# Kernel optimization log

Measured on AMD Instinct MI355X. Metric: run time of the kernel, lower is better.

The kernel has to match this reference:

```python
import jax, jax.numpy as jnp
import numpy as np

B, L, E, H, G, W, D = 2, 4096, 1024, 16, 2, 256, 64  # D = E // H; KV dim = E // (H // G)


def _rope(q, k, sin, cos):
    # Matches torch apply_rotary_pos_emb: split even/odd, concat halves (not interleaved).
    qe, qo = q[..., ::2], q[..., 1::2]
    ke, ko = k[..., ::2], k[..., 1::2]
    q_rot = jnp.concatenate([qe * cos - qo * sin, qe * sin + qo * cos], axis=-1)
    k_rot = jnp.concatenate([ke * cos - ko * sin, ke * sin + ko * cos], axis=-1)
    return q_rot, k_rot


def setup_inputs() -> dict:
    key = jax.random.key(0)
    ks = jax.random.split(key, 8)
    kv_dim = E // (H // G)  # 128
    s = 0.02
    return {
        "x": jax.random.normal(ks[0], (B, L, E), jnp.float32),
        "Wq1": jax.random.normal(ks[1], (E, E), jnp.float32) * s,
        "Wq2": jax.random.normal(ks[2], (E, E), jnp.float32) * s,
        "Wk1": jax.random.normal(ks[3], (E, kv_dim), jnp.float32) * s,
        "Wk2": jax.random.normal(ks[4], (E, kv_dim), jnp.float32) * s,
        "Wv": jax.random.normal(ks[5], (E, kv_dim), jnp.float32) * s,
        "Wout": jax.random.normal(ks[6], (E, E), jnp.float32) * s,
        "bout": jnp.zeros((E,), jnp.float32),
        "lq1": jnp.full((D,), 0.1, jnp.float32),
        "lk1": jnp.full((D,), 0.1, jnp.float32),
        "lq2": jnp.full((D,), -0.1, jnp.float32),
        "lk2": jnp.full((D,), -0.1, jnp.float32),
    }


def reference(x, Wq1, Wq2, Wk1, Wk2, Wv, Wout, bout, lq1, lk1, lq2, lk2):
    Bx, Lx, _ = x.shape  # Lx is a multiple of W -> pad_l = 0
    lambda_init = 0.8

    # Projections -> (B, H, L, D) and (B, G, L, D)
    q1 = (x @ Wq1).reshape(Bx, Lx, H, D).transpose(0, 2, 1, 3)
    q2 = (x @ Wq2).reshape(Bx, Lx, H, D).transpose(0, 2, 1, 3)
    k1 = (x @ Wk1).reshape(Bx, Lx, G, D).transpose(0, 2, 1, 3)
    k2 = (x @ Wk2).reshape(Bx, Lx, G, D).transpose(0, 2, 1, 3)
    v = (x @ Wv).reshape(Bx, Lx, G, D).transpose(0, 2, 1, 3)

    # RoPE tables (L, D/2) broadcast as (1, 1, L, D/2)
    pos = jnp.arange(Lx, dtype=jnp.float32)[:, None]
    div = jnp.exp(jnp.arange(0, D, 2, dtype=jnp.float32) * (-np.log(10000.0) / D))
    sin = jnp.sin(pos * div)[None, None]
    cos = jnp.cos(pos * div)[None, None]
    q1, k1 = _rope(q1, k1, sin, cos)
    q2, k2 = _rope(q2, k2, sin, cos)

    # Differential lambda (scalar), clamped to [0.1, 0.9]
    lam = jnp.clip(jnp.exp(lq1 @ lk1) - jnp.exp(lq2 @ lk2) + lambda_init, 0.1, 0.9)

    # KV repeat via torch .repeat(1, H//G, 1, 1): tiling -> head h uses group h % G
    gidx = jnp.arange(H) % G
    k1h, k2h, vh = k1[:, gidx], k2[:, gidx], v[:, gidx]  # (B, H, L, D)

    # Overlapping windows, stride W//2
    nw = (Lx - W) // (W // 2) + 1
    idx = jnp.arange(nw)[:, None] * (W // 2) + jnp.arange(W)[None, :]  # (nw, W)

    def win(t):
        return t[:, :, idx, :]  # (B, H, nw, W, D)

    scale = 1.0 / np.sqrt(D)

    def attn(qw, kw, vw):
        sc = jnp.einsum('bhnqd,bhnkd->bhnqk', qw, kw) * scale
        p = jax.nn.softmax(sc, axis=-1)  # bidirectional -> no causal mask
        return jnp.einsum('bhnqk,bhnkd->bhnqd', p, vw)

    a1 = attn(win(q1), win(k1h), win(vh))
    a2 = attn(win(q2), win(k2h), win(vh))
    a = a1 - lam * a2  # (B, H, nw, W, D)

    # Concatenate windows along seq (dim 2), transpose, flatten heads, trim to L
    a = a.reshape(Bx, H, nw * W, D).transpose(0, 2, 1, 3).reshape(Bx, nw * W, E)
    a = a[:, :Lx]
    return a @ Wout + bout
```

## Files before the change

### kernel.cpp

```cpp
#include <hip/hip_runtime.h>

#define SS    2176

typedef __bf16 bf16x8 __attribute__((ext_vector_type(8)));
typedef float floatx4 __attribute__((ext_vector_type(4)));
typedef const __attribute__((address_space(1))) void* as1cv;
typedef __attribute__((address_space(3))) void* as3v;

typedef uint4 __attribute__((may_alias, aligned(16))) uint4a;
typedef uint2 __attribute__((may_alias, aligned(8)))  uint2a;
typedef unsigned int __attribute__((may_alias)) uinta;

__device__ __forceinline__ float bf2f(unsigned short u) {
  unsigned int x = ((unsigned int)u) << 16;
  return __builtin_bit_cast(float, x);
}
__device__ __forceinline__ unsigned short f2bf(float f) {
  unsigned int u = __builtin_bit_cast(unsigned int, f);
  u = (u + 0x7fffu + ((u >> 16) & 1u)) >> 16;
  return (unsigned short)u;
}
#if __has_builtin(__builtin_amdgcn_cvt_pk_bf16_f32)
typedef __bf16 bf16x2 __attribute__((ext_vector_type(2)));
__device__ __forceinline__ unsigned int pk2bf(float a, float b) {
  bf16x2 r = __builtin_amdgcn_cvt_pk_bf16_f32(a, b);
  return __builtin_bit_cast(unsigned int, r);
}
#else
__device__ __forceinline__ unsigned int pk2bf(float a, float b) {
  return (unsigned int)f2bf(a) | ((unsigned int)f2bf(b) << 16);
}
#endif
__device__ __forceinline__ float fexp2(float x) {
#if __has_builtin(__builtin_amdgcn_exp2f)
  return __builtin_amdgcn_exp2f(x);
#else
  return exp2f(x);
#endif
}
__device__ __forceinline__ bf16x8 ld_frag(const unsigned short* p) {
  uint4 u = *(const uint4a*)p;
  return __builtin_bit_cast(bf16x8, u);
}
__device__ __forceinline__ bool sniff_bf16(const void* lq1) {
  return ((*(const uinta*)lq1) >> 16) == 0x3DCDu;
}
__device__ __forceinline__ float ldin(const void* p, int i, bool bf) {
  return bf ? bf2f(((const unsigned short*)p)[i]) : ((const float*)p)[i];
}

__global__ __launch_bounds__(256) void prep_kernel(
    const void* __restrict__ x,
    const void* __restrict__ Wq1, const void* __restrict__ Wq2,
    const void* __restrict__ Wk1, const void* __restrict__ Wk2,
    const void* __restrict__ Wv,  const void* __restrict__ Wout,
    const void* __restrict__ lq1, const void* __restrict__ lk1,
    const void* __restrict__ lq2, const void* __restrict__ lk2,
    unsigned short* __restrict__ WT, unsigned short* __restrict__ WoutT,
    float2* __restrict__ SC, float* __restrict__ lam_out,
    unsigned short* __restrict__ Xb)
{
  int bid = blockIdx.x, tid = threadIdx.x;
  bool bf = sniff_bf16(lq1);
  if (bid >= 1137) {
    int i = (bid - 1137) * 2048 + tid * 8;
    int r = i >> 10, c = i & 1023;
    size_t sidx = (size_t)(r + (r >= SS ? 1920 : 0)) * 1024 + c;
    if (bf) {
      *(uint4a*)(Xb + i) = *(const uint4a*)((const unsigned short*)x + sidx);
    } else {
      const float* xf = (const float*)x + sidx;
      uint4 o;
      o.x = pk2bf(xf[0], xf[1]); o.y = pk2bf(xf[2], xf[3]);
      o.z = pk2bf(xf[4], xf[5]); o.w = pk2bf(xf[6], xf[7]);
      *(uint4a*)(Xb + i) = o;
    }
  } else if (bid < 864) {
    __shared__ unsigned short T[64][80];
    const void* src; unsigned short* dst;
    int width, nloc, n0, k0;
    if (bid < 608) {
      n0 = (bid >> 4) * 64; k0 = (bid & 15) * 64; dst = WT;
      if      (n0 < 1024) { src = Wq1; width = 1024; nloc = n0; }
      else if (n0 < 2048) { src = Wq2; width = 1024; nloc = n0 - 1024; }
      else if (n0 < 2176) { src = Wk1; width = 128;  nloc = n0 - 2048; }
      else if (n0 < 2304) { src = Wk2; width = 128;  nloc = n0 - 2176; }
      else                { src = Wv;  width = 128;  nloc = n0 - 2304; }
    } else {
      int id = bid - 608;
      n0 = (id >> 4) * 64; k0 = (id & 15) * 64; dst = WoutT;
      src = Wout; width = 1024; nloc = n0;
    }
    for (int e = tid; e < 4096; e += 256) {
      int rr = e >> 6, cc = e & 63;
      size_t idx = (size_t)(k0 + rr) * width + nloc + cc;
      T[rr][cc] = bf ? ((const unsigned short*)src)[idx]
                     : f2bf(((const float*)src)[idx]);
    }
    __syncthreads();
#pragma unroll
    for (int it = 0; it < 2; ++it) {
      int rn = (tid >> 3) + it * 32;
      int ck = (tid & 7) * 8;
      unsigned short tmp[8] __attribute__((aligned(16)));
#pragma unroll
      for (int j = 0; j < 8; ++j) tmp[j] = T[ck + j][rn];
      *(uint4a*)(dst + (size_t)(n0 + rn) * 1024 + k0 + ck) = *(const uint4a*)tmp;
    }
  } else if (bid < 1136) {
    int idx = (bid - 864) * 256 + tid;
    int s = idx >> 5, j = idx & 31;
    float freq = expf(-(float)j * 0.28782313662425572f);
    float ang = (float)s * freq;
    SC[idx] = make_float2(sinf(ang), cosf(ang));
  } else {
    if (tid < 64) {
      float a = ldin(lq1, tid, bf) * ldin(lk1, tid, bf);
      float c = ldin(lq2, tid, bf) * ldin(lk2, tid, bf);
#pragma unroll
      for (int m = 32; m >= 1; m >>= 1) {
        a += __shfl_xor(a, m);
        c += __shfl_xor(c, m);
      }
      if (tid == 0) {
        float lam = expf(a) - expf(c) + 0.8f;
        lam = fminf(0.9f, fmaxf(0.1f, lam));
        *lam_out = lam;
      }
    }
  }
}

__global__ __launch_bounds__(256) void proj_gemm(
    const unsigned short* __restrict__ Xb, const unsigned short* __restrict__ WT,
    const float2* __restrict__ SC,
    unsigned short* __restrict__ Q1R, unsigned short* __restrict__ Q2R,
    unsigned short* __restrict__ K1R, unsigned short* __restrict__ K2R,
    unsigned short* __restrict__ VTg)
{
  __shared__ unsigned short As[128 * 32];
  __shared__ unsigned short Bs[128 * 32];
  int tid = threadIdx.x;
  int w = tid >> 6, lane = tid & 63, quad = lane >> 4, l15 = lane & 15;
  int wr = w >> 1, wc = w & 1;
  int n0 = blockIdx.x * 128, m0 = blockIdx.y * 128;
  int b = (m0 >= SS) ? 1 : 0;
  int srow = w * 32 + (lane >> 2);
  int scol = (((lane & 3) ^ ((lane >> 3) & 3))) * 8;
  int rch  = (quad ^ ((l15 >> 1) & 3)) * 8;

  floatx4 acc[4][4];
#pragma unroll
  for (int i = 0; i < 4; ++i)
#pragma unroll
    for (int j = 0; j < 4; ++j) acc[i][j] = (floatx4){0.f, 0.f, 0.f, 0.f};

  unsigned short* lA = As + (size_t)(w * 32) * 32;
  unsigned short* lB = Bs + (size_t)(w * 32) * 32;
  const unsigned short* gA = Xb + (size_t)(m0 + srow) * 1024 + scol;
  const unsigned short* gB = WT + (size_t)(n0 + srow) * 1024 + scol;

  for (int it = 0; it < 32; ++it) {
    int k0 = it * 32;
    __builtin_amdgcn_global_load_lds((as1cv)(gA + k0), (as3v)lA, 16, 0, 0);
    __builtin_amdgcn_global_load_lds((as1cv)(gA + 16 * 1024 + k0), (as3v)(lA + 16 * 32), 16, 0, 0);
    __builtin_amdgcn_global_load_lds((as1cv)(gB + k0), (as3v)lB, 16, 0, 0);
    __builtin_amdgcn_global_load_lds((as1cv)(gB + 16 * 1024 + k0), (as3v)(lB + 16 * 32), 16, 0, 0);
    __syncthreads();
    bf16x8 af[4], bfm[4];
#pragma unroll
    for (int rt = 0; rt < 4; ++rt)
      af[rt] = ld_frag(As + (size_t)(wr * 64 + rt * 16 + l15) * 32 + rch);
#pragma unroll
    for (int nt = 0; nt < 4; ++nt)
      bfm[nt] = ld_frag(Bs + (size_t)(wc * 64 + nt * 16 + l15) * 32 + rch);
#pragma unroll
    for (int rt = 0; rt < 4; ++rt)
#pragma unroll
      for (int nt = 0; nt < 4; ++nt)
        acc[rt][nt] = __builtin_amdgcn_mfma_f32_16x16x32_bf16(af[rt], bfm[nt], acc[rt][nt], 0, 0, 0);
    __syncthreads();
  }

  int seg, segbase;
  if      (n0 < 1024) { seg = 0; segbase = 0; }
  else if (n0 < 2048) { seg = 1; segbase = 1024; }
  else if (n0 < 2176) { seg = 2; segbase = 2048; }
  else if (n0 < 2304) { seg = 3; segbase = 2176; }
  else                { seg = 4; segbase = 2304; }
  int rb = m0 + wr * 64;

  if (seg == 4) {
#pragma unroll
    for (int rt = 0; rt < 4; ++rt) {
      int r = rb + rt * 16 + quad * 4;
      int s = r - b * SS;
#pragma unroll
      for (int nt = 0; nt < 4; ++nt) {
        int cs = n0 - segbase + wc * 64 + nt * 16 + l15;
        int gi = cs >> 6, dd = cs & 63;
        uint2 pk;
        pk.x = pk2bf(acc[rt][nt].x, acc[rt][nt].y);
        pk.y = pk2bf(acc[rt][nt].z, acc[rt][nt].w);
        *(uint2a*)(VTg + ((size_t)(b * 2 + gi) * 64 + dd) * SS + s) = pk;
      }
    }
  } else {
    unsigned short* dst = (seg == 0) ? Q1R : (seg == 1) ? Q2R : (seg == 2) ? K1R : K2R;
    bool isq = (seg <= 1);
    float oscale = isq ? 0.18033688011112042f : 1.0f;
#pragma unroll
    for (int rt = 0; rt < 4; ++rt) {
#pragma unroll
      for (int nt = 0; nt < 4; ++nt) {
        int cs = n0 - segbase + wc * 64 + nt * 16 + l15;
        int hh = cs >> 6, dd = cs & 63, j = dd >> 1, par = dd & 1;
        size_t tb = isq ? ((size_t)(b * 16 + hh) * SS) : ((size_t)(b * 2 + hh) * SS);
        int dloc = j + par * 32;
#pragma unroll
        for (int rg = 0; rg < 4; ++rg) {
          float v = acc[rt][nt][rg];
          float pv = __shfl_xor(v, 1);
          int r = rb + rt * 16 + quad * 4 + rg;
          int s = r - b * SS;
          float2 sc = SC[s * 32 + j];
          float o = par ? (pv * sc.x + v * sc.y) : (v * sc.y - pv * sc.x);
          dst[(tb + s) * 64 + dloc] = f2bf(o * oscale);
        }
      }
    }
  }
}

__global__ __launch_bounds__(512) void attn_kernel(
    const unsigned short* __restrict__ Q1R, const unsigned short* __restrict__ Q2R,
    const unsigned short* __restrict__ K1R, const unsigned short* __restrict__ K2R,
    const unsigned short* __restrict__ VTg, const float* __restrict__ lamp,
    unsigned short* __restrict__ Abuf)
{
  __shared__ unsigned short K1s[256 * 64];
  __shared__ unsigned short K2s[256 * 64];
  __shared__ unsigned short VTs[64 * 256];
  __shared__ unsigned short P[8][2][32 * 40];
  int nx = blockIdx.x, hp = blockIdx.y, b = blockIdx.z;
  int n = nx >> 1, qh = nx & 1;
  int g = hp & 1, hpair = hp >> 1;
  int tid = threadIdx.x, w = tid >> 6, lane = tid & 63, quad = lane >> 4, l15 = lane & 15;
  int wq = w & 3;
  int h = g + 4 * hpair + 2 * (w >> 2);
  int s0 = n * 128;
  int qbase = s0 + qh * 128 + wq * 32;

  const unsigned short* q1b = Q1R + (size_t)(b * 16 + h) * SS * 64;
  const unsigned short* q2b = Q2R + (size_t)(b * 16 + h) * SS * 64;
  const unsigned short* k1w = K1R + ((size_t)(b * 2 + g) * SS + s0) * 64;
  const unsigned short* k2w = K2R + ((size_t)(b * 2 + g) * SS + s0) * 64;
  const unsigned short* vtw = VTg + (size_t)(b * 2 + g) * 64 * SS + s0;

#pragma unroll
  for (int i = 0; i < 4; ++i) {
    int r = i * 64 + (tid >> 3);
    int cg = (tid & 7) ^ (r & 7);
    __builtin_amdgcn_global_load_lds((as1cv)(k1w + r * 64 + cg * 8),
        (as3v)(K1s + i * 4096 + tid * 8), 16, 0, 0);
    __builtin_amdgcn_global_load_lds((as1cv)(k2w + r * 64 + cg * 8),
        (as3v)(K2s + i * 4096 + tid * 8), 16, 0, 0);
  }
#pragma unroll
  for (int i = 0; i < 4; ++i) {
    int d = i * 16 + (tid >> 5);
    int cg = (tid & 31) ^ (d & 7);
    __builtin_amdgcn_global_load_lds((as1cv)(vtw + (size_t)d * SS + cg * 8),
        (as3v)(VTs + i * 4096 + tid * 8), 16, 0, 0);
  }

  bf16x8 q1f[2][2], q2f[2][2];
#pragma unroll
  for (int rt = 0; rt < 2; ++rt) {
    int sq = qbase + rt * 16 + l15;
#pragma unroll
    for (int kt = 0; kt < 2; ++kt) {
      q1f[rt][kt] = ld_frag(q1b + (size_t)sq * 64 + kt * 32 + quad * 8);
      q2f[rt][kt] = ld_frag(q2b + (size_t)sq * 64 + kt * 32 + quad * 8);
    }
  }
  float lam = *lamp;

  floatx4 O1[2][4], O2[2][4];
  float l1s[2] = {0.f, 0.f}, l2s[2] = {0.f, 0.f};
#pragma unroll
  for (int rt = 0; rt < 2; ++rt)
#pragma unroll
    for (int dt = 0; dt < 4; ++dt) {
      O1[rt][dt] = (floatx4){0.f, 0.f, 0.f, 0.f};
      O2[rt][dt] = (floatx4){0.f, 0.f, 0.f, 0.f};
    }

  __syncthreads();

  for (int c = 0; c < 4; ++c) {
#pragma unroll
    for (int ntp = 0; ntp < 2; ++ntp) {
      int kbl = c * 64 + ntp * 32;
      bf16x8 k1f[2][2], k2f[2][2], vb[4];
#pragma unroll
      for (int ntl = 0; ntl < 2; ++ntl) {
        int kl = kbl + ntl * 16 + l15;
#pragma unroll
        for (int kt = 0; kt < 2; ++kt) {
          int slot = (kt * 4 + quad) ^ (kl & 7);
          k1f[ntl][kt] = ld_frag(K1s + kl * 64 + slot * 8);
          k2f[ntl][kt] = ld_frag(K2s + kl * 64 + slot * 8);
        }
      }
#pragma unroll
      for (int dt = 0; dt < 4; ++dt) {
        int d = dt * 16 + l15;
        int slot = ((kbl >> 3) + quad) ^ (d & 7);
        vb[dt] = ld_frag(VTs + d * 256 + slot * 8);
      }

#pragma unroll
      for (int rt = 0; rt < 2; ++rt)
#pragma unroll
        for (int ntl = 0; ntl < 2; ++ntl) {
          floatx4 sa = (floatx4){0.f, 0.f, 0.f, 0.f};
          sa = __builtin_amdgcn_mfma_f32_16x16x32_bf16(k1f[ntl][0], q1f[rt][0], sa, 0, 0, 0);
          sa = __builtin_amdgcn_mfma_f32_16x16x32_bf16(k1f[ntl][1], q1f[rt][1], sa, 0, 0, 0);
          floatx4 pe;
          pe.x = fexp2(sa.x); pe.y = fexp2(sa.y);
          pe.z = fexp2(sa.z); pe.w = fexp2(sa.w);
          l1s[rt] += (pe.x + pe.y) + (pe.z + pe.w);
          uint2 dw; dw.x = pk2bf(pe.x, pe.y); dw.y = pk2bf(pe.z, pe.w);
          *(uint2a*)&P[w][0][(rt * 16 + l15) * 40 + ntl * 16 + quad * 4] = dw;
        }
#pragma unroll
      for (int rt = 0; rt < 2; ++rt)
#pragma unroll
        for (int ntl = 0; ntl < 2; ++ntl) {
          floatx4 sa = (floatx4){0.f, 0.f, 0.f, 0.f};
          sa = __builtin_amdgcn_mfma_f32_16x16x32_bf16(k2f[ntl][0], q2f[rt][0], sa, 0, 0, 0);
          sa = __builtin_amdgcn_mfma_f32_16x16x32_bf16(k2f[ntl][1], q2f[rt][1], sa, 0, 0, 0);
          floatx4 pe;
          pe.x = fexp2(sa.x); pe.y = fexp2(sa.y);
          pe.z = fexp2(sa.z); pe.w = fexp2(sa.w);
          l2s[rt] += (pe.x + pe.y) + (pe.z + pe.w);
          uint2 dw; dw.x = pk2bf(pe.x, pe.y); dw.y = pk2bf(pe.z, pe.w);
          *(uint2a*)&P[w][1][(rt * 16 + l15) * 40 + ntl * 16 + quad * 4] = dw;
        }
#pragma unroll
      for (int rt = 0; rt < 2; ++rt) {
        bf16x8 pa = ld_frag(&P[w][0][(rt * 16 + l15) * 40 + quad * 8]);
#pragma unroll
        for (int dt = 0; dt < 4; ++dt)
          O1[rt][dt] = __builtin_amdgcn_mfma_f32_16x16x32_bf16(pa, vb[dt], O1[rt][dt], 0, 0, 0);
      }
#pragma unroll
      for (int rt = 0; rt < 2; ++rt) {
        bf16x8 pa = ld_frag(&P[w][1][(rt * 16 + l15) * 40 + quad * 8]);
#pragma unroll
        for (int dt = 0; dt < 4; ++dt)
          O2[rt][dt] = __builtin_amdgcn_mfma_f32_16x16x32_bf16(pa, vb[dt], O2[rt][dt], 0, 0, 0);
      }
    }
  }

#pragma unroll
  for (int rt = 0; rt < 2; ++rt) {
    l1s[rt] += __shfl_xor(l1s[rt], 16); l1s[rt] += __shfl_xor(l1s[rt], 32);
    l2s[rt] += __shfl_xor(l2s[rt], 16); l2s[rt] += __shfl_xor(l2s[rt], 32);
  }

#pragma unroll
  for (int rt = 0; rt < 2; ++rt) {
    floatx4 r1, r2;
#pragma unroll
    for (int rg = 0; rg < 4; ++rg) {
      int src = (lane & 48) | (quad * 4 + rg);
      r1[rg] = 1.f / __shfl(l1s[rt], src);
      r2[rg] = lam / __shfl(l2s[rt], src);
    }
#pragma unroll
    for (int dt = 0; dt < 4; ++dt) {
#pragma unroll
      for (int rg = 0; rg < 4; ++rg) {
        float v = O1[rt][dt][rg] * r1[rg] - O2[rt][dt][rg] * r2[rg];
        int prow = n * 256 + qh * 128 + wq * 32 + rt * 16 + quad * 4 + rg;
        int col = h * 64 + dt * 16 + l15;
        Abuf[((size_t)b * 4096 + prow) * 1024 + col] = f2bf(v);
      }
    }
  }
}

__global__ __launch_bounds__(256) void out_gemm(
    const unsigned short* __restrict__ A, const unsigned short* __restrict__ WoutT,
    const void* __restrict__ bout, const void* __restrict__ lq1,
    void* __restrict__ out)
{
  __shared__ unsigned short As[128 * 32];
  __shared__ unsigned short Bs[128 * 32];
  int tid = threadIdx.x;
  int w = tid >> 6, lane = tid & 63, quad = lane >> 4, l15 = lane & 15;
  int wr = w >> 1, wc = w & 1;
  int n0 = blockIdx.x * 128, m0 = blockIdx.y * 128;
  int srow = w * 32 + (lane >> 2);
  int scol = (((lane & 3) ^ ((lane >> 3) & 3))) * 8;
  int rch  = (quad ^ ((l15 >> 1) & 3)) * 8;
  bool bf = sniff_bf16(lq1);

  floatx4 acc[4][4];
#pragma unroll
  for (int i = 0; i < 4; ++i)
#pragma unroll
    for (int j = 0; j < 4; ++j) acc[i][j] = (floatx4){0.f, 0.f, 0.f, 0.f};

  unsigned short* lA = As + (size_t)(w * 32) * 32;
  unsigned short* lB = Bs + (size_t)(w * 32) * 32;
  const unsigned short* gA = A + (size_t)(m0 + srow) * 1024 + scol;
  const unsigned short* gB = WoutT + (size_t)(n0 + srow) * 1024 + scol;

  for (int it = 0; it < 32; ++it) {
    int k0 = it * 32;
    __builtin_amdgcn_global_load_lds((as1cv)(gA + k0), (as3v)lA, 16, 0, 0);
    __builtin_amdgcn_global_load_lds((as1cv)(gA + 16 * 1024 + k0), (as3v)(lA + 16 * 32), 16, 0, 0);
    __builtin_amdgcn_global_load_lds((as1cv)(gB + k0), (as3v)lB, 16, 0, 0);
    __builtin_amdgcn_global_load_lds((as1cv)(gB + 16 * 1024 + k0), (as3v)(lB + 16 * 32), 16, 0, 0);
    __syncthreads();
    bf16x8 af[4], bfm[4];
#pragma unroll
    for (int rt = 0; rt < 4; ++rt)
      af[rt] = ld_frag(As + (size_t)(wr * 64 + rt * 16 + l15) * 32 + rch);
#pragma unroll
    for (int nt = 0; nt < 4; ++nt)
      bfm[nt] = ld_frag(Bs + (size_t)(wc * 64 + nt * 16 + l15) * 32 + rch);
#pragma unroll
    for (int rt = 0; rt < 4; ++rt)
#pragma unroll
      for (int nt = 0; nt < 4; ++nt)
        acc[rt][nt] = __builtin_amdgcn_mfma_f32_16x16x32_bf16(af[rt], bfm[nt], acc[rt][nt], 0, 0, 0);
    __syncthreads();
  }

#pragma unroll
  for (int rt = 0; rt < 4; ++rt)
#pragma unroll
    for (int nt = 0; nt < 4; ++nt) {
      int cc = n0 + wc * 64 + nt * 16 + l15;
      float bias = ldin(bout, cc, bf);
#pragma unroll
      for (int rg = 0; rg < 4; ++rg) {
        int r = m0 + wr * 64 + rt * 16 + quad * 4 + rg;
        float v = acc[rt][nt][rg] + bias;
        if (bf) ((unsigned short*)out)[(size_t)r * 1024 + cc] = f2bf(v);
        else    ((float*)out)[(size_t)r * 1024 + cc] = v;
      }
    }
}

extern "C" void kernel_launch(void* const* d_in, const int* in_sizes, int n_in,
                              void* d_out, int out_size, void* d_ws, size_t ws_size,
                              hipStream_t stream) {
  (void)in_sizes; (void)n_in; (void)out_size; (void)ws_size;
  const void* x    = d_in[0];
  const void* Wq1  = d_in[1];
  const void* Wq2  = d_in[2];
  const void* Wk1  = d_in[3];
  const void* Wk2  = d_in[4];
  const void* Wv   = d_in[5];
  const void* Wout = d_in[6];
  const void* bout = d_in[7];
  const void* lq1  = d_in[8];
  const void* lk1  = d_in[9];
  const void* lq2  = d_in[10];
  const void* lk2  = d_in[11];

  char* ws = (char*)d_ws;
  unsigned short* WT    = (unsigned short*)(ws + 0);
  unsigned short* WoutT = (unsigned short*)(ws + 4980736);
  float2*         SC    = (float2*)(ws + 7077888);
  float*          lam   = (float*)(ws + 7634944);
  unsigned short* Q1R   = (unsigned short*)(ws + 7635200);
  unsigned short* Q2R   = (unsigned short*)(ws + 16548096);
  unsigned short* K1R   = (unsigned short*)(ws + 25460992);
  unsigned short* K2R   = (unsigned short*)(ws + 26575104);
  unsigned short* VTg   = (unsigned short*)(ws + 27689216);
  unsigned short* Abuf  = (unsigned short*)(ws + 28803328);
  unsigned short* Xb    = (unsigned short*)(ws + 45580544);

  prep_kernel<<<3313, 256, 0, stream>>>(x, Wq1, Wq2, Wk1, Wk2, Wv, Wout,
                                        lq1, lk1, lq2, lk2, WT, WoutT, SC, lam, Xb);
  proj_gemm<<<dim3(19, 34), 256, 0, stream>>>(Xb, WT, SC, Q1R, Q2R, K1R, K2R, VTg);
  attn_kernel<<<dim3(32, 8, 2), 512, 0, stream>>>(Q1R, Q2R, K1R, K2R, VTg, lam, Abuf);
  out_gemm<<<dim3(8, 64), 256, 0, stream>>>(Abuf, WoutT, bout, lq1, (unsigned short*)d_out);
}
```

Before: 222.8 us.

## Double-buffer LDS tiles in projection and output GEMMs to overlap loads with MFMA

The projection and output GEMM kernels now keep two LDS stages for A and B. The global-to-LDS load for the next K-tile is issued before the MFMA work on the current tile, with a prologue that preloads the first tile. The goal is to hide global memory latency behind matrix compute instead of stalling on a barrier right after each load. This doubles LDS use per block, which could reduce occupancy, and it relies on the trailing per-iteration barrier to wait for the async loads.

```diff
diff --git a/kernel.cpp b/kernel.cpp
--- a/kernel.cpp
+++ b/kernel.cpp
@@ -138,8 +138,8 @@
     unsigned short* __restrict__ K1R, unsigned short* __restrict__ K2R,
     unsigned short* __restrict__ VTg)
 {
-  __shared__ unsigned short As[128 * 32];
-  __shared__ unsigned short Bs[128 * 32];
+  __shared__ unsigned short As[2][128 * 32];
+  __shared__ unsigned short Bs[2][128 * 32];
   int tid = threadIdx.x;
   int w = tid >> 6, lane = tid & 63, quad = lane >> 4, l15 = lane & 15;
   int wr = w >> 1, wc = w & 1;
@@ -155,25 +155,32 @@
 #pragma unroll
     for (int j = 0; j < 4; ++j) acc[i][j] = (floatx4){0.f, 0.f, 0.f, 0.f};
 
-  unsigned short* lA = As + (size_t)(w * 32) * 32;
-  unsigned short* lB = Bs + (size_t)(w * 32) * 32;
+  int wb = w * 32 * 32;
   const unsigned short* gA = Xb + (size_t)(m0 + srow) * 1024 + scol;
   const unsigned short* gB = WT + (size_t)(n0 + srow) * 1024 + scol;
 
+  __builtin_amdgcn_global_load_lds((as1cv)gA, (as3v)(As[0] + wb), 16, 0, 0);
+  __builtin_amdgcn_global_load_lds((as1cv)(gA + 16 * 1024), (as3v)(As[0] + wb + 16 * 32), 16, 0, 0);
+  __builtin_amdgcn_global_load_lds((as1cv)gB, (as3v)(Bs[0] + wb), 16, 0, 0);
+  __builtin_amdgcn_global_load_lds((as1cv)(gB + 16 * 1024), (as3v)(Bs[0] + wb + 16 * 32), 16, 0, 0);
+  __syncthreads();
+
   for (int it = 0; it < 32; ++it) {
-    int k0 = it * 32;
-    __builtin_amdgcn_global_load_lds((as1cv)(gA + k0), (as3v)lA, 16, 0, 0);
-    __builtin_amdgcn_global_load_lds((as1cv)(gA + 16 * 1024 + k0), (as3v)(lA + 16 * 32), 16, 0, 0);
-    __builtin_amdgcn_global_load_lds((as1cv)(gB + k0), (as3v)lB, 16, 0, 0);
-    __builtin_amdgcn_global_load_lds((as1cv)(gB + 16 * 1024 + k0), (as3v)(lB + 16 * 32), 16, 0, 0);
-    __syncthreads();
+    int cur = it & 1;
+    if (it < 31) {
+      int k1 = (it + 1) * 32;
+      __builtin_amdgcn_global_load_lds((as1cv)(gA + k1), (as3v)(As[cur ^ 1] + wb), 16, 0, 0);
+      __builtin_amdgcn_global_load_lds((as1cv)(gA + 16 * 1024 + k1), (as3v)(As[cur ^ 1] + wb + 16 * 32), 16, 0, 0);
+      __builtin_amdgcn_global_load_lds((as1cv)(gB + k1), (as3v)(Bs[cur ^ 1] + wb), 16, 0, 0);
+      __builtin_amdgcn_global_load_lds((as1cv)(gB + 16 * 1024 + k1), (as3v)(Bs[cur ^ 1] + wb + 16 * 32), 16, 0, 0);
+    }
     bf16x8 af[4], bfm[4];
 #pragma unroll
     for (int rt = 0; rt < 4; ++rt)
-      af[rt] = ld_frag(As + (size_t)(wr * 64 + rt * 16 + l15) * 32 + rch);
+      af[rt] = ld_frag(As[cur] + (size_t)(wr * 64 + rt * 16 + l15) * 32 + rch);
 #pragma unroll
     for (int nt = 0; nt < 4; ++nt)
-      bfm[nt] = ld_frag(Bs + (size_t)(wc * 64 + nt * 16 + l15) * 32 + rch);
+      bfm[nt] = ld_frag(Bs[cur] + (size_t)(wc * 64 + nt * 16 + l15) * 32 + rch);
 #pragma unroll
     for (int rt = 0; rt < 4; ++rt)
 #pragma unroll
@@ -398,8 +405,8 @@
     const void* __restrict__ bout, const void* __restrict__ lq1,
     void* __restrict__ out)
 {
-  __shared__ unsigned short As[128 * 32];
-  __shared__ unsigned short Bs[128 * 32];
+  __shared__ unsigned short As[2][128 * 32];
+  __shared__ unsigned short Bs[2][128 * 32];
   int tid = threadIdx.x;
   int w = tid >> 6, lane = tid & 63, quad = lane >> 4, l15 = lane & 15;
   int wr = w >> 1, wc = w & 1;
@@ -415,25 +422,32 @@
 #pragma unroll
     for (int j = 0; j < 4; ++j) acc[i][j] = (floatx4){0.f, 0.f, 0.f, 0.f};
 
-  unsigned short* lA = As + (size_t)(w * 32) * 32;
-  unsigned short* lB = Bs + (size_t)(w * 32) * 32;
+  int wb = w * 32 * 32;
   const unsigned short* gA = A + (size_t)(m0 + srow) * 1024 + scol;
   const unsigned short* gB = WoutT + (size_t)(n0 + srow) * 1024 + scol;
 
+  __builtin_amdgcn_global_load_lds((as1cv)gA, (as3v)(As[0] + wb), 16, 0, 0);
+  __builtin_amdgcn_global_load_lds((as1cv)(gA + 16 * 1024), (as3v)(As[0] + wb + 16 * 32), 16, 0, 0);
+  __builtin_amdgcn_global_load_lds((as1cv)gB, (as3v)(Bs[0] + wb), 16, 0, 0);
+  __builtin_amdgcn_global_load_lds((as1cv)(gB + 16 * 1024), (as3v)(Bs[0] + wb + 16 * 32), 16, 0, 0);
+  __syncthreads();
+
   for (int it = 0; it < 32; ++it) {
-    int k0 = it * 32;
-    __builtin_amdgcn_global_load_lds((as1cv)(gA + k0), (as3v)lA, 16, 0, 0);
-    __builtin_amdgcn_global_load_lds((as1cv)(gA + 16 * 1024 + k0), (as3v)(lA + 16 * 32), 16, 0, 0);
-    __builtin_amdgcn_global_load_lds((as1cv)(gB + k0), (as3v)lB, 16, 0, 0);
-    __builtin_amdgcn_global_load_lds((as1cv)(gB + 16 * 1024 + k0), (as3v)(lB + 16 * 32), 16, 0, 0);
-    __syncthreads();
+    int cur = it & 1;
+    if (it < 31) {
+      int k1 = (it + 1) * 32;
+      __builtin_amdgcn_global_load_lds((as1cv)(gA + k1), (as3v)(As[cur ^ 1] + wb), 16, 0, 0);
+      __builtin_amdgcn_global_load_lds((as1cv)(gA + 16 * 1024 + k1), (as3v)(As[cur ^ 1] + wb + 16 * 32), 16, 0, 0);
+      __builtin_amdgcn_global_load_lds((as1cv)(gB + k1), (as3v)(Bs[cur ^ 1] + wb), 16, 0, 0);
+      __builtin_amdgcn_global_load_lds((as1cv)(gB + 16 * 1024 + k1), (as3v)(Bs[cur ^ 1] + wb + 16 * 32), 16, 0, 0);
+    }
     bf16x8 af[4], bfm[4];
 #pragma unroll
     for (int rt = 0; rt < 4; ++rt)
-      af[rt] = ld_frag(As + (size_t)(wr * 64 + rt * 16 + l15) * 32 + rch);
+      af[rt] = ld_frag(As[cur] + (size_t)(wr * 64 + rt * 16 + l15) * 32 + rch);
 #pragma unroll
     for (int nt = 0; nt < 4; ++nt)
-      bfm[nt] = ld_frag(Bs + (size_t)(wc * 64 + nt * 16 + l15) * 32 + rch);
+      bfm[nt] = ld_frag(Bs[cur] + (size_t)(wc * 64 + nt * 16 + l15) * 32 + rch);
 #pragma unroll
     for (int rt = 0; rt < 4; ++rt)
 #pragma unroll
```

Measured after the change: 234.5 us. 5.3% more time.
